# Optimization experiments

Hardware: AMD Instinct MI355X
Metric: run time of the kernel (lower is better)

## Reference

```python
import jax, jax.numpy as jnp
import numpy as np

B, I, H = 32768, 128, 128


def setup_inputs() -> dict:
    key = jax.random.key(0)
    ks = jax.random.split(key, 11)
    s = 1.0 / np.sqrt(H)
    return {
        "x": jax.random.normal(ks[0], (B, I), jnp.float32),
        "h": jax.random.normal(ks[1], (B, H), jnp.float32),
        "c": jax.random.normal(ks[2], (B, H), jnp.float32),
        "W1": jax.random.normal(ks[3], (H, I + H), jnp.float32) * s,
        "b1": jax.random.normal(ks[4], (H,), jnp.float32) * s + 1.0,  # forget-gate bias offset 1.0
        "W2": jax.random.normal(ks[5], (H, I + H), jnp.float32) * s,
        "b2": jax.random.normal(ks[6], (H,), jnp.float32) * s,
        "Wf": jax.random.normal(ks[7], (H, I + H), jnp.float32) * s,
        "bf": jax.random.normal(ks[8], (H,), jnp.float32) * s,
        "W3": jax.random.normal(ks[9], (H, I + H), jnp.float32) * s,
        "b3": jax.random.normal(ks[10], (H,), jnp.float32) * s,
    }


def reference(x, h, c, W1, b1, W2, b2, Wf, bf, W3, b3):
    # total_in = inp + hidden (coordinate-list concat == feature concat)
    total = jnp.concatenate([x, h], axis=-1)  # [B, I+H]
    sig1 = jax.nn.sigmoid(total @ W1.T + b1)  # forget gate (bias offset +1)
    sig2 = jax.nn.sigmoid(total @ W2.T + b2)  # input gate
    f_l = jnp.tanh(total @ Wf.T + bf)         # candidate via symmetric f
    sig3 = jax.nn.sigmoid(total @ W3.T + b3)  # output gate
    new_c = c * sig1 + sig2 * f_l             # fused elementwise combine
    new_h = jnp.tanh(new_c) * sig3
    return new_h, new_c
```

## Files before the change

### kernel.cpp

```cpp
#include <hip/hip_runtime.h>

#define B_TOTAL 32768
#define NROWB   128
#define TILE    16
#define NT      8

typedef __attribute__((ext_vector_type(8)))  short    bf16x8;
typedef __attribute__((ext_vector_type(4)))  float    f32x4;
typedef __attribute__((ext_vector_type(4)))  unsigned u32x4;

__device__ __forceinline__ unsigned rne1(float f) {
    unsigned u = __builtin_bit_cast(unsigned, f);
    return (u + 0x7FFFu + ((u >> 16) & 1u)) >> 16;
}
__device__ __forceinline__ unsigned cvtpk(float lo, float hi) {
    unsigned r;
    asm("v_cvt_pk_bf16_f32 %0, %1, %2" : "=v"(r) : "v"(lo), "v"(hi));
    return r;
}
__device__ __forceinline__ float fsig(float v) {
    return __fdividef(1.0f, 1.0f + __expf(-v));
}
__device__ __forceinline__ float ftanh(float v) {
    return 1.0f - __fdividef(2.0f, 1.0f + __expf(2.0f * v));
}

__global__ void wconv_kernel(const float* __restrict__ w1, const float* __restrict__ w2,
                             const float* __restrict__ wf, const float* __restrict__ w3,
                             u32x4* __restrict__ out) {
    int T = blockIdx.x * 256 + threadIdx.x;
    int F = T >> 6, l = T & 63;
    int s = F >> 4, tau = (F >> 3) & 1, ks = F & 7;
    int n16 = l & 15;
    int g = n16 & 3, hl = n16 >> 2;
    const float* W = (g == 0) ? w1 : (g == 1) ? w2 : (g == 2) ? wf : w3;
    const float* src = W + (s * 8 + tau * 4 + hl) * 256 + ks * 32 + (l >> 4) * 8;
    f32x4 lo = *(const f32x4*)src;
    f32x4 hi = *(const f32x4*)(src + 4);
    u32x4 r;
    r[0] = rne1(lo[0]) | (rne1(lo[1]) << 16);
    r[1] = rne1(lo[2]) | (rne1(lo[3]) << 16);
    r[2] = rne1(hi[0]) | (rne1(hi[1]) << 16);
    r[3] = rne1(hi[2]) | (rne1(hi[3]) << 16);
    out[T] = r;
}

__global__ __launch_bounds__(512, 4) void lstm_kernel(
    const float* __restrict__ x, const float* __restrict__ h, const float* __restrict__ c,
    const bf16x8* __restrict__ wfrag,
    const float* __restrict__ b1, const float* __restrict__ b2,
    const float* __restrict__ bfv, const float* __restrict__ b3,
    float* __restrict__ out)
{
    __shared__ __align__(16) char smem[2][TILE * 1024];

    const int tid  = threadIdx.x;
    const int wave = tid >> 6;
    const int lane = tid & 63;
    const int rb   = lane & 15;
    const int c4   = lane >> 4;
    const int cg   = blockIdx.x & 1;
    const long row0 = (long)(blockIdx.x >> 1) * NROWB;
    const int s    = cg * 8 + wave;
    const int col0 = s * 8 + c4;
    const int col1 = col0 + 4;

    auto STAGE = [&](int t) {
        char* buf = smem[t & 1];
        const long gr0 = row0 + (long)t * TILE;
#pragma unroll
        for (int i = 0; i < 2; ++i) {
            const int r = wave * 2 + i;
            const unsigned kb = ((unsigned)lane * 16u) ^ (((unsigned)r & 7u) << 4);
            const float* src = (kb < 512u)
                ? (x + (gr0 + r) * 128 + (kb >> 2))
                : (h + (gr0 + r) * 128 + ((kb - 512u) >> 2));
            __builtin_amdgcn_global_load_lds(
                (const __attribute__((address_space(1))) unsigned*)src,
                (__attribute__((address_space(3))) unsigned*)(buf + r * 1024),
                16, 0, 0);
        }
    };

    STAGE(0);

    bf16x8 wfr[2][8];
#pragma unroll
    for (int tau = 0; tau < 2; ++tau)
#pragma unroll
        for (int ks = 0; ks < 8; ++ks)
            wfr[tau][ks] = wfrag[(size_t)((s * 2 + tau) * 8 + ks) * 64 + lane];

    f32x4 bias[2];
    bias[0] = (f32x4){ b1[col0], b2[col0], bfv[col0], b3[col0] };
    bias[1] = (f32x4){ b1[col1], b2[col1], bfv[col1], b3[col1] };

    float* out_h = out;
    float* out_c = out + (size_t)B_TOTAL * 128;

#pragma unroll 1
    for (int t = 0; t < NT; ++t) {
        __syncthreads();

        const long gr0 = row0 + (long)t * TILE;
        const float* crow = c + (gr0 + rb) * 128;
        const float cv0 = crow[col0];
        const float cv1 = crow[col1];

        if (t + 1 < NT) STAGE(t + 1);

        const char* buf = smem[t & 1];

        f32x4 acc[2] = { bias[0], bias[1] };

#pragma unroll
        for (int ks = 0; ks < 8; ++ks) {
            const unsigned swz = ((unsigned)rb & 7u) << 4;
            const unsigned kb  = (unsigned)(ks * 128 + c4 * 32);
            const char* p = buf + rb * 1024;
            f32x4 a0 = *(const f32x4*)(p + (kb ^ swz));
            f32x4 a1 = *(const f32x4*)(p + ((kb + 16u) ^ swz));
            union { unsigned u[4]; bf16x8 v; } pk;
            pk.u[0] = cvtpk(a0[0], a0[1]);
            pk.u[1] = cvtpk(a0[2], a0[3]);
            pk.u[2] = cvtpk(a1[0], a1[1]);
            pk.u[3] = cvtpk(a1[2], a1[3]);
            acc[0] = __builtin_amdgcn_mfma_f32_16x16x32_bf16(wfr[0][ks], pk.v, acc[0], 0, 0, 0);
            acc[1] = __builtin_amdgcn_mfma_f32_16x16x32_bf16(wfr[1][ks], pk.v, acc[1], 0, 0, 0);
        }

        const long orow = (gr0 + rb) * 128;
#pragma unroll
        for (int tau = 0; tau < 2; ++tau) {
            const float G1 = fsig(acc[tau][0]);
            const float G2 = fsig(acc[tau][1]);
            const float GF = ftanh(acc[tau][2]);
            const float G3 = fsig(acc[tau][3]);
            const float cv = tau ? cv1 : cv0;
            const float nc = cv * G1 + G2 * GF;
            const float nh = ftanh(nc) * G3;
            const int colt = tau ? col1 : col0;
            out_h[orow + colt] = nh;
            out_c[orow + colt] = nc;
        }
    }
}

extern "C" void kernel_launch(void* const* d_in, const int* in_sizes, int n_in,
                              void* d_out, int out_size, void* d_ws, size_t ws_size,
                              hipStream_t stream) {
    (void)in_sizes; (void)n_in; (void)out_size; (void)ws_size;
    const float* x  = (const float*)d_in[0];
    const float* h  = (const float*)d_in[1];
    const float* c  = (const float*)d_in[2];
    const float* W1 = (const float*)d_in[3];
    const float* b1 = (const float*)d_in[4];
    const float* W2 = (const float*)d_in[5];
    const float* b2 = (const float*)d_in[6];
    const float* Wf = (const float*)d_in[7];
    const float* bf = (const float*)d_in[8];
    const float* W3 = (const float*)d_in[9];
    const float* b3 = (const float*)d_in[10];

    wconv_kernel<<<64, 256, 0, stream>>>(W1, W2, Wf, W3, (u32x4*)d_ws);
    lstm_kernel<<<B_TOTAL / NROWB * 2, 512, 0, stream>>>(
        x, h, c, (const bf16x8*)d_ws, b1, b2, bf, b3, (float*)d_out);
}
```

Before: 40.01 us.

## Replace LDS staging with per-wave register prefetch of activations and split columns four ways

Drops the shared-memory double buffer, its global_load_lds staging and the per-tile __syncthreads. Each wave now loads its own x and h fragments straight into registers and prefetches the next half-tile while the current one is converted and fed to MFMA. Work is split so four 256-thread blocks cover each 128-row strip, each wave owning one 8-column slice. The cost is that every row of x and h is fetched by 16 waves instead of being shared through LDS, which adds L1/L2 traffic and register pressure in exchange for removing block-level synchronisation.

```diff
diff --git a/kernel.cpp b/kernel.cpp
--- a/kernel.cpp
+++ b/kernel.cpp
@@ -1,9 +1,8 @@
 #include <hip/hip_runtime.h>
 
 #define B_TOTAL 32768
-#define NROWB   128
+#define STRIP   128
 #define TILE    16
-#define NT      8
 
 typedef __attribute__((ext_vector_type(8)))  short    bf16x8;
 typedef __attribute__((ext_vector_type(4)))  float    f32x4;
@@ -45,103 +44,110 @@
     out[T] = r;
 }
 
-__global__ __launch_bounds__(512, 4) void lstm_kernel(
+__global__ __launch_bounds__(256, 3) void lstm_kernel(
     const float* __restrict__ x, const float* __restrict__ h, const float* __restrict__ c,
     const bf16x8* __restrict__ wfrag,
     const float* __restrict__ b1, const float* __restrict__ b2,
     const float* __restrict__ bfv, const float* __restrict__ b3,
     float* __restrict__ out)
 {
-    __shared__ __align__(16) char smem[2][TILE * 1024];
-
     const int tid  = threadIdx.x;
     const int wave = tid >> 6;
     const int lane = tid & 63;
     const int rb   = lane & 15;
     const int c4   = lane >> 4;
-    const int cg   = blockIdx.x & 1;
-    const long row0 = (long)(blockIdx.x >> 1) * NROWB;
-    const int s    = cg * 8 + wave;
-    const int col0 = s * 8 + c4;
+    const int S    = (blockIdx.x & 3) * 4 + wave;
+    const long strip0 = (long)(blockIdx.x >> 2) * STRIP;
+    const int col0 = S * 8 + c4;
     const int col1 = col0 + 4;
 
-    auto STAGE = [&](int t) {
-        char* buf = smem[t & 1];
-        const long gr0 = row0 + (long)t * TILE;
+    f32x4 raw[8];
+    auto ISSUE = [&](long r0, int half) {
+        const float* src = (half ? h : x) + (r0 + rb) * 128 + c4 * 8;
 #pragma unroll
-        for (int i = 0; i < 2; ++i) {
-            const int r = wave * 2 + i;
-            const unsigned kb = ((unsigned)lane * 16u) ^ (((unsigned)r & 7u) << 4);
-            const float* src = (kb < 512u)
-                ? (x + (gr0 + r) * 128 + (kb >> 2))
-                : (h + (gr0 + r) * 128 + ((kb - 512u) >> 2));
-            __builtin_amdgcn_global_load_lds(
-                (const __attribute__((address_space(1))) unsigned*)src,
-                (__attribute__((address_space(3))) unsigned*)(buf + r * 1024),
-                16, 0, 0);
+        for (int k2 = 0; k2 < 4; ++k2) {
+            raw[k2 * 2]     = *(const f32x4*)(src + k2 * 32);
+            raw[k2 * 2 + 1] = *(const f32x4*)(src + k2 * 32 + 4);
         }
     };
 
-    STAGE(0);
+    ISSUE(strip0, 0);
 
     bf16x8 wfr[2][8];
 #pragma unroll
     for (int tau = 0; tau < 2; ++tau)
 #pragma unroll
         for (int ks = 0; ks < 8; ++ks)
-            wfr[tau][ks] = wfrag[(size_t)((s * 2 + tau) * 8 + ks) * 64 + lane];
+            wfr[tau][ks] = wfrag[(size_t)((S * 2 + tau) * 8 + ks) * 64 + lane];
 
-    f32x4 bias[2];
-    bias[0] = (f32x4){ b1[col0], b2[col0], bfv[col0], b3[col0] };
-    bias[1] = (f32x4){ b1[col1], b2[col1], bfv[col1], b3[col1] };
+    const f32x4 bias0 = (f32x4){ b1[col0], b2[col0], bfv[col0], b3[col0] };
+    const f32x4 bias1 = (f32x4){ b1[col1], b2[col1], bfv[col1], b3[col1] };
 
     float* out_h = out;
     float* out_c = out + (size_t)B_TOTAL * 128;
 
 #pragma unroll 1
-    for (int t = 0; t < NT; ++t) {
-        __syncthreads();
-
-        const long gr0 = row0 + (long)t * TILE;
+    for (int t = 0; t < STRIP / TILE; ++t) {
+        const long gr0 = strip0 + t * TILE;
         const float* crow = c + (gr0 + rb) * 128;
         const float cv0 = crow[col0];
         const float cv1 = crow[col1];
 
-        if (t + 1 < NT) STAGE(t + 1);
-
-        const char* buf = smem[t & 1];
-
-        f32x4 acc[2] = { bias[0], bias[1] };
+        f32x4 acc0 = bias0, acc1 = bias1;
+        bf16x8 hb[4];
 
 #pragma unroll
-        for (int ks = 0; ks < 8; ++ks) {
-            const unsigned swz = ((unsigned)rb & 7u) << 4;
-            const unsigned kb  = (unsigned)(ks * 128 + c4 * 32);
-            const char* p = buf + rb * 1024;
-            f32x4 a0 = *(const f32x4*)(p + (kb ^ swz));
-            f32x4 a1 = *(const f32x4*)(p + ((kb + 16u) ^ swz));
+        for (int k2 = 0; k2 < 4; ++k2) {
             union { unsigned u[4]; bf16x8 v; } pk;
-            pk.u[0] = cvtpk(a0[0], a0[1]);
-            pk.u[1] = cvtpk(a0[2], a0[3]);
-            pk.u[2] = cvtpk(a1[0], a1[1]);
-            pk.u[3] = cvtpk(a1[2], a1[3]);
-            acc[0] = __builtin_amdgcn_mfma_f32_16x16x32_bf16(wfr[0][ks], pk.v, acc[0], 0, 0, 0);
-            acc[1] = __builtin_amdgcn_mfma_f32_16x16x32_bf16(wfr[1][ks], pk.v, acc[1], 0, 0, 0);
+            pk.u[0] = cvtpk(raw[2 * k2][0],     raw[2 * k2][1]);
+            pk.u[1] = cvtpk(raw[2 * k2][2],     raw[2 * k2][3]);
+            pk.u[2] = cvtpk(raw[2 * k2 + 1][0], raw[2 * k2 + 1][1]);
+            pk.u[3] = cvtpk(raw[2 * k2 + 1][2], raw[2 * k2 + 1][3]);
+            hb[k2] = pk.v;
+        }
+        ISSUE(gr0, 1);
+#pragma unroll
+        for (int k2 = 0; k2 < 4; ++k2) {
+            acc0 = __builtin_amdgcn_mfma_f32_16x16x32_bf16(wfr[0][k2], hb[k2], acc0, 0, 0, 0);
+            acc1 = __builtin_amdgcn_mfma_f32_16x16x32_bf16(wfr[1][k2], hb[k2], acc1, 0, 0, 0);
+        }
+
+#pragma unroll
+        for (int k2 = 0; k2 < 4; ++k2) {
+            union { unsigned u[4]; bf16x8 v; } pk;
+            pk.u[0] = cvtpk(raw[2 * k2][0],     raw[2 * k2][1]);
+            pk.u[1] = cvtpk(raw[2 * k2][2],     raw[2 * k2][3]);
+            pk.u[2] = cvtpk(raw[2 * k2 + 1][0], raw[2 * k2 + 1][1]);
+            pk.u[3] = cvtpk(raw[2 * k2 + 1][2], raw[2 * k2 + 1][3]);
+            hb[k2] = pk.v;
+        }
+        if (t + 1 < STRIP / TILE) ISSUE(gr0 + TILE, 0);
+#pragma unroll
+        for (int k2 = 0; k2 < 4; ++k2) {
+            acc0 = __builtin_amdgcn_mfma_f32_16x16x32_bf16(wfr[0][4 + k2], hb[k2], acc0, 0, 0, 0);
+            acc1 = __builtin_amdgcn_mfma_f32_16x16x32_bf16(wfr[1][4 + k2], hb[k2], acc1, 0, 0, 0);
         }
 
         const long orow = (gr0 + rb) * 128;
-#pragma unroll
-        for (int tau = 0; tau < 2; ++tau) {
-            const float G1 = fsig(acc[tau][0]);
-            const float G2 = fsig(acc[tau][1]);
-            const float GF = ftanh(acc[tau][2]);
-            const float G3 = fsig(acc[tau][3]);
-            const float cv = tau ? cv1 : cv0;
-            const float nc = cv * G1 + G2 * GF;
+        {
+            const float G1 = fsig(acc0[0]);
+            const float G2 = fsig(acc0[1]);
+            const float GF = ftanh(acc0[2]);
+            const float G3 = fsig(acc0[3]);
+            const float nc = cv0 * G1 + G2 * GF;
             const float nh = ftanh(nc) * G3;
-            const int colt = tau ? col1 : col0;
-            out_h[orow + colt] = nh;
-            out_c[orow + colt] = nc;
+            out_h[orow + col0] = nh;
+            out_c[orow + col0] = nc;
+        }
+        {
+            const float G1 = fsig(acc1[0]);
+            const float G2 = fsig(acc1[1]);
+            const float GF = ftanh(acc1[2]);
+            const float G3 = fsig(acc1[3]);
+            const float nc = cv1 * G1 + G2 * GF;
+            const float nh = ftanh(nc) * G3;
+            out_h[orow + col1] = nh;
+            out_c[orow + col1] = nc;
         }
     }
 }
@@ -163,6 +169,6 @@
     const float* b3 = (const float*)d_in[10];
 
     wconv_kernel<<<64, 256, 0, stream>>>(W1, W2, Wf, W3, (u32x4*)d_ws);
-    lstm_kernel<<<B_TOTAL / NROWB * 2, 512, 0, stream>>>(
+    lstm_kernel<<<(B_TOTAL / STRIP) * 4, 256, 0, stream>>>(
         x, h, c, (const bf16x8*)d_ws, b1, b2, bf, b3, (float*)d_out);
 }
```

Result: slower. 85.28 us (+113.1%).
